# Performance work log

Measured on AMD Instinct MI355X. Metric: run time of the kernel, lower is better.

The kernel has to match this reference:

```python
import jax, jax.numpy as jnp
import numpy as np

B, T, N, H = 32, 512, 32, 128  # batch, time, num_series (== num_chans), hidden


def setup_inputs() -> dict:
    key = jax.random.key(0)
    ks = jax.random.split(key, 7)
    s = 1.0 / np.sqrt(H)  # PyTorch LSTM default init range
    X = jax.random.normal(ks[0], (B, T, N), dtype=jnp.float32)
    W_ih = jax.random.uniform(ks[1], (N, 4 * H, N), minval=-s, maxval=s, dtype=jnp.float32)
    W_hh = jax.random.uniform(ks[2], (N, 4 * H, H), minval=-s, maxval=s, dtype=jnp.float32)
    b_ih = jax.random.uniform(ks[3], (N, 4 * H), minval=-s, maxval=s, dtype=jnp.float32)
    b_hh = jax.random.uniform(ks[4], (N, 4 * H), minval=-s, maxval=s, dtype=jnp.float32)
    W_out = jax.random.uniform(ks[5], (N, H), minval=-s, maxval=s, dtype=jnp.float32)  # Conv1d(hidden,1,1) weight per series
    b_out = jax.random.uniform(ks[6], (N,), minval=-s, maxval=s, dtype=jnp.float32)
    return dict(X=X, W_ih=W_ih, W_hh=W_hh, b_ih=b_ih, b_hh=b_hh, W_out=W_out, b_out=b_out)


def reference(X, W_ih, W_hh, b_ih, b_hh, W_out, b_out):
    """Ensemble of N independent single-layer LSTMs over the same input X,
    each followed by a 1x1 conv (linear) head; outputs concatenated on dim 2.
    Gate order follows PyTorch: i, f, g, o."""
    Bsz, Tlen, P = X.shape
    Nser, _, Hid = W_hh.shape
    # Precompute input projections for all series/timesteps: [T, N, B, 4H]
    xproj = jnp.einsum('btp,ngp->tnbg', X, W_ih) + (b_ih + b_hh)[None, :, None, :]
    h0 = jnp.zeros((Nser, Bsz, Hid), X.dtype)
    c0 = jnp.zeros((Nser, Bsz, Hid), X.dtype)

    def step(carry, xt):
        h, c = carry
        gates = xt + jnp.einsum('nbh,ngh->nbg', h, W_hh)  # [N,B,4H]
        i, f, g, o = jnp.split(gates, 4, axis=-1)
        c = jax.nn.sigmoid(f) * c + jax.nn.sigmoid(i) * jnp.tanh(g)
        h = jax.nn.sigmoid(o) * jnp.tanh(c)
        return (h, c), h

    (hT, cT), hs = jax.lax.scan(step, (h0, c0), xproj)  # hs: [T, N, B, H]
    # 1x1 conv head per series, then concatenate along series dim -> [B, T, N]
    pred = jnp.einsum('tnbh,nh->btn', hs, W_out) + b_out[None, None, :]
    return pred, hT, cT
```

## Files before the change

kernel.cpp:

```cpp
#include <hip/hip_runtime.h>
#include <hip/hip_bf16.h>

typedef __attribute__((ext_vector_type(8))) short s16x8;
typedef __attribute__((ext_vector_type(4))) float f32x4;

#define MFMA_B16(a, b, c) __builtin_amdgcn_mfma_f32_16x16x32_bf16((a), (b), (c), 0, 0, 0)

static __device__ __forceinline__ short f2bf(float f) {
    __hip_bfloat16 h = __float2bfloat16(f);
    return __builtin_bit_cast(short, h);
}
static __device__ __forceinline__ float rcp_f(float x) {
    return __builtin_amdgcn_rcpf(x);
}

__global__ void xcvt_kernel(const float* __restrict__ X, short* __restrict__ Xb, int n) {
    int i = (blockIdx.x * 256 + threadIdx.x) * 4;
    if (i < n) {
        float4 v = *(const float4*)(X + i);
        short4 o;
        o.x = f2bf(v.x); o.y = f2bf(v.y); o.z = f2bf(v.z); o.w = f2bf(v.w);
        *(short4*)(Xb + i) = o;
    }
}

template<bool BF16X>
__global__ __launch_bounds__(512, 2)
void clstm_kernel(const float* __restrict__ X,
                  const short* __restrict__ Xb,
                  const float* __restrict__ W_ih,
                  const float* __restrict__ W_hh,
                  const float* __restrict__ b_ih,
                  const float* __restrict__ b_hh,
                  const float* __restrict__ W_out,
                  const float* __restrict__ b_out,
                  float* __restrict__ out)
{
    constexpr int B = 32, T = 512, N = 32, H = 128, G = 512;
    constexpr int HT_OFF = B * T * N;
    constexpr int CT_OFF = HT_OFF + N * B * H;
    constexpr int PRED_OFF = 8192;
    constexpr float C1 = 1.4426950408889634f;

    __shared__ __align__(16) unsigned char smem[16384];

    const int tid  = threadIdx.x;
    const int w    = tid >> 6;
    const int L    = tid & 63;
    const int col  = L & 15;
    const int quad = L >> 4;
    const int n    = blockIdx.x & 31;
    const int bgrp = blockIdx.x >> 5;

    s16x8 Bh[4][4];
    s16x8 Bx[4];
    f32x4 biasv[4];
#pragma unroll
    for (int tt = 0; tt < 4; ++tt) {
        const int g = (w + 8 * tt) * 16 + col;
        const float* whr = W_hh + ((size_t)n * G + g) * H + quad * 8;
#pragma unroll
        for (int kt = 0; kt < 4; ++kt) {
            const float* p = whr + kt * 32;
#pragma unroll
            for (int jj = 0; jj < 8; ++jj) Bh[tt][kt][jj] = f2bf(p[jj]);
        }
        const float* wir = W_ih + ((size_t)n * G + g) * N + quad * 8;
#pragma unroll
        for (int jj = 0; jj < 8; ++jj) Bx[tt][jj] = f2bf(wir[jj]);
        const float bb = b_ih[n * G + g] + b_hh[n * G + g];
        biasv[tt] = (f32x4){bb, bb, bb, bb};
    }

    s16x8 Bp[4];
    const float bo = b_out[n];
    const f32x4 bov = (f32x4){bo, bo, bo, bo};
#pragma unroll
    for (int kt = 0; kt < 4; ++kt) {
        const float* wp = W_out + n * H + kt * 32 + quad * 8;
#pragma unroll
        for (int jj = 0; jj < 8; ++jj)
            Bp[kt][jj] = (col == 0) ? f2bf(wp[jj]) : (short)0;
    }

    int wboff;
    {
        const int j = w * 16 + col;
        wboff = (j >> 5) * 1024 + (((((j >> 3) & 3) << 4) | (quad << 2)) * 16) + (j & 7) * 2;
    }

    const bool xactive = (col & 3) == 0;
    const int  xb      = bgrp * 4 + (col >> 2);
    const float* xp  = X + ((size_t)xb * T) * N + quad * 8;
    const short* xbp = BF16X ? (Xb + ((size_t)xb * T) * N + quad * 8) : nullptr;

    auto loadx = [&](int t) -> s16x8 {
        s16x8 r = (s16x8)(short)0;
        if (xactive) {
            if constexpr (BF16X) {
                r = *(const s16x8*)(xbp + (size_t)t * N);
            } else {
                float4 lo = *(const float4*)(xp + (size_t)t * N);
                float4 hi = *(const float4*)(xp + (size_t)t * N + 4);
                r[0] = f2bf(lo.x); r[1] = f2bf(lo.y); r[2] = f2bf(lo.z); r[3] = f2bf(lo.w);
                r[4] = f2bf(hi.x); r[5] = f2bf(hi.y); r[6] = f2bf(hi.z); r[7] = f2bf(hi.w);
            }
        }
        return r;
    };

    *(float4*)(smem + tid * 16)        = make_float4(0.f, 0.f, 0.f, 0.f);
    *(float4*)(smem + 8192 + tid * 16) = make_float4(0.f, 0.f, 0.f, 0.f);

    float cst = 0.f, hlast = 0.f;

    f32x4 accN[4];
    {
        s16x8 x0 = loadx(0);
#pragma unroll
        for (int tt = 0; tt < 4; ++tt)
            accN[tt] = MFMA_B16(x0, Bx[tt], biasv[tt]);
    }
    s16x8 xA = loadx(1);
    s16x8 xB = loadx(2);

    __syncthreads();

#define STEP(P, TCUR)                                                               \
    {                                                                               \
        const unsigned char* rb = smem + (P) * 4096;                                \
        s16x8 Af[4];                                                                \
        _Pragma("unroll")                                                           \
        for (int kt = 0; kt < 4; ++kt)                                              \
            Af[kt] = *(const s16x8*)(rb + kt * 1024 + L * 16);                      \
        f32x4 acc[4];                                                               \
        _Pragma("unroll")                                                           \
        for (int tt = 0; tt < 4; ++tt) acc[tt] = accN[tt];                          \
        _Pragma("unroll")                                                           \
        for (int kt = 0; kt < 4; ++kt) {                                            \
            _Pragma("unroll")                                                       \
            for (int tt = 0; tt < 4; ++tt)                                          \
                acc[tt] = MFMA_B16(Af[kt], Bh[tt][kt], acc[tt]);                    \
        }                                                                           \
        if (w == ((TCUR) & 7)) {                                                    \
            f32x4 pacc = bov;                                                       \
            _Pragma("unroll")                                                       \
            for (int kt = 0; kt < 4; ++kt)                                          \
                pacc = MFMA_B16(Af[kt], Bp[kt], pacc);                              \
            if ((TCUR) > 0 && col == 0)                                             \
                *(float*)(smem + PRED_OFF + ((quad << 9) + (TCUR) - 1) * 4) =       \
                    pacc[0];                                                        \
        }                                                                           \
                         \
        _Pragma("unroll")                                                           \
        for (int tt = 0; tt < 4; ++tt)                                              \
            accN[tt] = MFMA_B16(xA, Bx[tt], biasv[tt]);                             \
        xA = xB;                                                                    \
        xB = loadx(((TCUR) + 3 < T) ? (TCUR) + 3 : T - 1);                          \
                                     \
        {                                                                           \
            const float iv = acc[0][0], fv = acc[1][0];                             \
            const float gv = acc[2][0], ov = acc[3][0];                             \
            const float ei = exp2f(-C1 * iv);                                       \
            const float ef = exp2f(-C1 * fv);                                       \
            const float eg = exp2f(-2.0f * C1 * gv);                                \
            const float eo = exp2f(-C1 * ov);                                       \
            const float sf = rcp_f(1.0f + ef);                                      \
            const float itg = (1.0f - eg) * rcp_f((1.0f + ei) * (1.0f + eg));       \
            const float cc = __builtin_fmaf(sf, cst, itg);                          \
            cst = cc;                                                               \
            const float ec = exp2f(-2.0f * C1 * cc);                                \
            const float hv = (1.0f - ec) * rcp_f((1.0f + eo) * (1.0f + ec));        \
            hlast = hv;                                                             \
            *(short*)(smem + ((P) ^ 1) * 4096 + wboff) = f2bf(hv);                  \
        }                                                                           \
        __syncthreads();                                                            \
    }

#pragma unroll 1
    for (int t2 = 0; t2 < T; t2 += 2) {
        STEP(0, t2)
        STEP(1, t2 + 1)
    }
#undef STEP

    if (w == 0) {
        f32x4 pacc = bov;
#pragma unroll
        for (int kt = 0; kt < 4; ++kt) {
            s16x8 Af = *(const s16x8*)(smem + kt * 1024 + L * 16);
            pacc = MFMA_B16(Af, Bp[kt], pacc);
        }
        if (col == 0)
            *(float*)(smem + PRED_OFF + ((quad << 9) + (T - 1)) * 4) = pacc[0];
    }
    __syncthreads();

#pragma unroll
    for (int e = tid; e < 4 * T; e += 512) {
        const int b = e >> 9, t = e & (T - 1);
        out[((size_t)(bgrp * 4 + b) * T + t) * N + n] =
            *(const float*)(smem + PRED_OFF + e * 4);
    }

    {
        const int bglob = bgrp * 4 + quad;
        const int j = w * 16 + col;
        out[HT_OFF + ((size_t)n * B + bglob) * H + j] = hlast;
        out[CT_OFF + ((size_t)n * B + bglob) * H + j] = cst;
    }
}

extern "C" void kernel_launch(void* const* d_in, const int* in_sizes, int n_in,
                              void* d_out, int out_size, void* d_ws, size_t ws_size,
                              hipStream_t stream) {
    const float* X     = (const float*)d_in[0];
    const float* W_ih  = (const float*)d_in[1];
    const float* W_hh  = (const float*)d_in[2];
    const float* b_ih  = (const float*)d_in[3];
    const float* b_hh  = (const float*)d_in[4];
    const float* W_out = (const float*)d_in[5];
    const float* b_out = (const float*)d_in[6];
    float* out = (float*)d_out;

    const int xelems = 32 * 512 * 32;
    const bool usebf = ws_size >= (size_t)xelems * sizeof(short);

    if (usebf) {
        short* Xb = (short*)d_ws;
        xcvt_kernel<<<dim3(xelems / 1024), dim3(256), 0, stream>>>(X, Xb, xelems);
        clstm_kernel<true><<<dim3(256), dim3(512), 0, stream>>>(
            X, Xb, W_ih, W_hh, b_ih, b_hh, W_out, b_out, out);
    } else {
        clstm_kernel<false><<<dim3(256), dim3(512), 0, stream>>>(
            X, nullptr, W_ih, W_hh, b_ih, b_hh, W_out, b_out, out);
    }
}
```

Measured before the change: 365.9 us.

## Halve workgroup to 4 waves, each wave computing two hidden-column tiles per step

Each workgroup drops from 8 to 4 wavefronts, and each wave now handles two 16-column hidden slices. That doubles the MFMA tiles, the weight registers and the gate math per wave. The aim is to make the per-timestep __syncthreads barrier cheaper with fewer waves and to give each wave more independent MFMA work to hide latency. In exchange, register pressure roughly doubles (32 Bh fragments) and the per-wave serial chain per step gets longer, since each step's MFMA work now sits on half as many waves.

```diff
diff --git a/kernel.cpp b/kernel.cpp
--- a/kernel.cpp
+++ b/kernel.cpp
@@ -25,7 +25,7 @@
 }
 
 template<bool BF16X>
-__global__ __launch_bounds__(512, 2)
+__global__ __launch_bounds__(256, 1)
 void clstm_kernel(const float* __restrict__ X,
                   const short* __restrict__ Xb,
                   const float* __restrict__ W_ih,
@@ -52,12 +52,13 @@
     const int n    = blockIdx.x & 31;
     const int bgrp = blockIdx.x >> 5;
 
-    s16x8 Bh[4][4];
-    s16x8 Bx[4];
-    f32x4 biasv[4];
-#pragma unroll
-    for (int tt = 0; tt < 4; ++tt) {
-        const int g = (w + 8 * tt) * 16 + col;
+    s16x8 Bh[8][4];
+    s16x8 Bx[8];
+    f32x4 biasv[8];
+#pragma unroll
+    for (int tt = 0; tt < 8; ++tt) {
+        const int type = tt >> 1, jp = tt & 1;
+        const int g = (type * 8 + jp * 4 + w) * 16 + col;
         const float* whr = W_hh + ((size_t)n * G + g) * H + quad * 8;
 #pragma unroll
         for (int kt = 0; kt < 4; ++kt) {
@@ -83,11 +84,11 @@
             Bp[kt][jj] = (col == 0) ? f2bf(wp[jj]) : (short)0;
     }
 
-    int wboff;
-    {
-        const int j = w * 16 + col;
-        wboff = (j >> 5) * 1024 + (((((j >> 3) & 3) << 4) | (quad << 2)) * 16) + (j & 7) * 2;
-    }
+    auto mkoff = [&](int j) {
+        return (j >> 5) * 1024 + (((((j >> 3) & 3) << 4) | (quad << 2)) * 16) + (j & 7) * 2;
+    };
+    const int wboff0 = mkoff(w * 16 + col);
+    const int wboff1 = mkoff((w + 4) * 16 + col);
 
     const bool xactive = (col & 3) == 0;
     const int  xb      = bgrp * 4 + (col >> 2);
@@ -109,16 +110,17 @@
         return r;
     };
 
-    *(float4*)(smem + tid * 16)        = make_float4(0.f, 0.f, 0.f, 0.f);
-    *(float4*)(smem + 8192 + tid * 16) = make_float4(0.f, 0.f, 0.f, 0.f);
-
-    float cst = 0.f, hlast = 0.f;
-
-    f32x4 accN[4];
+#pragma unroll
+    for (int i = tid; i < 1024; i += 256)
+        ((float4*)smem)[i] = make_float4(0.f, 0.f, 0.f, 0.f);
+
+    float cst0 = 0.f, hlast0 = 0.f, cst1 = 0.f, hlast1 = 0.f;
+
+    f32x4 accN[8];
     {
         s16x8 x0 = loadx(0);
 #pragma unroll
-        for (int tt = 0; tt < 4; ++tt)
+        for (int tt = 0; tt < 8; ++tt)
             accN[tt] = MFMA_B16(x0, Bx[tt], biasv[tt]);
     }
     s16x8 xA = loadx(1);
@@ -133,16 +135,16 @@
         _Pragma("unroll")                                                           \
         for (int kt = 0; kt < 4; ++kt)                                              \
             Af[kt] = *(const s16x8*)(rb + kt * 1024 + L * 16);                      \
-        f32x4 acc[4];                                                               \
-        _Pragma("unroll")                                                           \
-        for (int tt = 0; tt < 4; ++tt) acc[tt] = accN[tt];                          \
+        f32x4 acc[8];                                                               \
+        _Pragma("unroll")                                                           \
+        for (int tt = 0; tt < 8; ++tt) acc[tt] = accN[tt];                          \
         _Pragma("unroll")                                                           \
         for (int kt = 0; kt < 4; ++kt) {                                            \
             _Pragma("unroll")                                                       \
-            for (int tt = 0; tt < 4; ++tt)                                          \
+            for (int tt = 0; tt < 8; ++tt)                                          \
                 acc[tt] = MFMA_B16(Af[kt], Bh[tt][kt], acc[tt]);                    \
         }                                                                           \
-        if (w == ((TCUR) & 7)) {                                                    \
+        if (w == ((TCUR) & 3)) {                                                    \
             f32x4 pacc = bov;                                                       \
             _Pragma("unroll")                                                       \
             for (int kt = 0; kt < 4; ++kt)                                          \
@@ -153,26 +155,34 @@
         }                                                                           \
                          \
         _Pragma("unroll")                                                           \
-        for (int tt = 0; tt < 4; ++tt)                                              \
+        for (int tt = 0; tt < 8; ++tt)                                              \
             accN[tt] = MFMA_B16(xA, Bx[tt], biasv[tt]);                             \
         xA = xB;                                                                    \
         xB = loadx(((TCUR) + 3 < T) ? (TCUR) + 3 : T - 1);                          \
-                                     \
+                     \
         {                                                                           \
-            const float iv = acc[0][0], fv = acc[1][0];                             \
-            const float gv = acc[2][0], ov = acc[3][0];                             \
-            const float ei = exp2f(-C1 * iv);                                       \
-            const float ef = exp2f(-C1 * fv);                                       \
-            const float eg = exp2f(-2.0f * C1 * gv);                                \
-            const float eo = exp2f(-C1 * ov);                                       \
-            const float sf = rcp_f(1.0f + ef);                                      \
-            const float itg = (1.0f - eg) * rcp_f((1.0f + ei) * (1.0f + eg));       \
-            const float cc = __builtin_fmaf(sf, cst, itg);                          \
-            cst = cc;                                                               \
-            const float ec = exp2f(-2.0f * C1 * cc);                                \
-            const float hv = (1.0f - ec) * rcp_f((1.0f + eo) * (1.0f + ec));        \
-            hlast = hv;                                                             \
-            *(short*)(smem + ((P) ^ 1) * 4096 + wboff) = f2bf(hv);                  \
+            const float iv0 = acc[0][0], fv0 = acc[2][0];                           \
+            const float gv0 = acc[4][0], ov0 = acc[6][0];                           \
+            const float iv1 = acc[1][0], fv1 = acc[3][0];                           \
+            const float gv1 = acc[5][0], ov1 = acc[7][0];                           \
+            const float ei0 = exp2f(-C1 * iv0), ei1 = exp2f(-C1 * iv1);             \
+            const float ef0 = exp2f(-C1 * fv0), ef1 = exp2f(-C1 * fv1);             \
+            const float eg0 = exp2f(-2.0f * C1 * gv0), eg1 = exp2f(-2.0f * C1 * gv1); \
+            const float eo0 = exp2f(-C1 * ov0), eo1 = exp2f(-C1 * ov1);             \
+            const float sf0 = rcp_f(1.0f + ef0), sf1 = rcp_f(1.0f + ef1);           \
+            const float itg0 = (1.0f - eg0) * rcp_f((1.0f + ei0) * (1.0f + eg0));   \
+            const float itg1 = (1.0f - eg1) * rcp_f((1.0f + ei1) * (1.0f + eg1));   \
+            const float cc0 = __builtin_fmaf(sf0, cst0, itg0);                      \
+            const float cc1 = __builtin_fmaf(sf1, cst1, itg1);                      \
+            cst0 = cc0; cst1 = cc1;                                                 \
+            const float ec0 = exp2f(-2.0f * C1 * cc0);                              \
+            const float ec1 = exp2f(-2.0f * C1 * cc1);                              \
+            const float hv0 = (1.0f - ec0) * rcp_f((1.0f + eo0) * (1.0f + ec0));    \
+            const float hv1 = (1.0f - ec1) * rcp_f((1.0f + eo1) * (1.0f + ec1));    \
+            hlast0 = hv0; hlast1 = hv1;                                             \
+            unsigned char* wbb = smem + ((P) ^ 1) * 4096;                           \
+            *(short*)(wbb + wboff0) = f2bf(hv0);                                    \
+            *(short*)(wbb + wboff1) = f2bf(hv1);                                    \
         }                                                                           \
         __syncthreads();                                                            \
     }
@@ -197,7 +207,7 @@
     __syncthreads();
 
 #pragma unroll
-    for (int e = tid; e < 4 * T; e += 512) {
+    for (int e = tid; e < 4 * T; e += 256) {
         const int b = e >> 9, t = e & (T - 1);
         out[((size_t)(bgrp * 4 + b) * T + t) * N + n] =
             *(const float*)(smem + PRED_OFF + e * 4);
@@ -205,9 +215,12 @@
 
     {
         const int bglob = bgrp * 4 + quad;
-        const int j = w * 16 + col;
-        out[HT_OFF + ((size_t)n * B + bglob) * H + j] = hlast;
-        out[CT_OFF + ((size_t)n * B + bglob) * H + j] = cst;
+        const int j0 = w * 16 + col;
+        const int j1 = (w + 4) * 16 + col;
+        out[HT_OFF + ((size_t)n * B + bglob) * H + j0] = hlast0;
+        out[CT_OFF + ((size_t)n * B + bglob) * H + j0] = cst0;
+        out[HT_OFF + ((size_t)n * B + bglob) * H + j1] = hlast1;
+        out[CT_OFF + ((size_t)n * B + bglob) * H + j1] = cst1;
     }
 }
 
@@ -229,10 +242,10 @@
     if (usebf) {
         short* Xb = (short*)d_ws;
         xcvt_kernel<<<dim3(xelems / 1024), dim3(256), 0, stream>>>(X, Xb, xelems);
-        clstm_kernel<true><<<dim3(256), dim3(512), 0, stream>>>(
+        clstm_kernel<true><<<dim3(256), dim3(256), 0, stream>>>(
             X, Xb, W_ih, W_hh, b_ih, b_hh, W_out, b_out, out);
     } else {
-        clstm_kernel<false><<<dim3(256), dim3(512), 0, stream>>>(
+        clstm_kernel<false><<<dim3(256), dim3(256), 0, stream>>>(
             X, nullptr, W_ih, W_hh, b_ih, b_hh, W_out, b_out, out);
     }
 }
```

Measured after the change: 449.8 us. 1.23x slower.
